# Optimization experiments

Measured on AMD Instinct MI355X. Metric: run time of the kernel, lower is better.

Reference implementation:

```python
import jax, jax.numpy as jnp
import numpy as np

NEG = -1e9

def setup_inputs() -> dict:
    key = jax.random.key(0)
    k1, k2, k3, k4, k5 = jax.random.split(key, 5)
    B, S, D = 4, 2048, 1024
    x = jax.random.normal(k1, (B, S, D), dtype=jnp.float32)
    Wq = jax.random.normal(k2, (D, D), dtype=jnp.float32) * (1.0 / np.sqrt(D))
    Wk = jax.random.normal(k3, (D, D), dtype=jnp.float32) * (1.0 / np.sqrt(D))
    Wv = jax.random.normal(k4, (D, D), dtype=jnp.float32) * (1.0 / np.sqrt(D))
    mask = jax.random.randint(k5, (B, S), 0, 2) > 0  # bool [B,S]
    return {"x": x, "Wq": Wq, "Wk": Wk, "Wv": Wv, "mask": mask}

def reference(x, Wq, Wk, Wv, mask):
    # x: [B,S,D]; single-head self-attention, scale = 1/sqrt(D)
    D = x.shape[-1]
    scale = 1.0 / D ** 0.5
    q = jnp.einsum('bsi,ij->bsj', x, Wq)
    k = jnp.einsum('bsi,ij->bsj', x, Wk)
    y = jnp.einsum('bsi,bzi->bsz', q, k) * scale  # [B,S,S]
    # additive mask: (~mask)[:, :, None] * -1e9 broadcasts over key axis
    m = (~mask).astype(jnp.float32)[:, :, None]
    y = y + m * NEG
    v = jnp.einsum('bsi,ij->bsj', x, Wv)
    attn = jax.nn.softmax(y, axis=-1)
    return jnp.einsum('bsz,bzi->bsi', attn, v)
```

## Files before the change

### kernel.cpp

```cpp
#include <hip/hip_runtime.h>

typedef __bf16 bf16x8 __attribute__((ext_vector_type(8)));
typedef float f32x4 __attribute__((ext_vector_type(4)));
typedef unsigned short u16;

__device__ __forceinline__ u16 f2bf(float f) {
    union { float f; unsigned u; } v; v.f = f;
    unsigned r = (v.u + 0x7FFFu + ((v.u >> 16) & 1u)) >> 16;
    return (u16)r;
}

__device__ __forceinline__ void fence_bar() {
    asm volatile("" ::: "memory");
    __builtin_amdgcn_s_barrier();
    asm volatile("" ::: "memory");
}

__global__ __launch_bounds__(256)
void normMask(const unsigned int* __restrict__ m, unsigned char* __restrict__ nm) {
    __shared__ int isByte;
    if (threadIdx.x == 0) isByte = 0;
    __syncthreads();
    int bad = 0;
    for (int i = threadIdx.x; i < 2048; i += 256) bad |= (m[i] > 1u);
    if (bad) atomicOr(&isByte, 1);
    __syncthreads();
    if (isByte) {
        const unsigned char* mb = (const unsigned char*)m;
        for (int i = threadIdx.x; i < 8192; i += 256) nm[i] = mb[i] ? 1 : 0;
    } else {
        for (int i = threadIdx.x; i < 8192; i += 256) nm[i] = (unsigned char)m[i];
    }
}

__global__ __launch_bounds__(256)
void transW(const float* __restrict__ Wq, const float* __restrict__ Wk,
            const float* __restrict__ Wv, u16* __restrict__ Wt) {
    __shared__ u16 tile[64][65];
    const float* W = blockIdx.z == 0 ? Wq : (blockIdx.z == 1 ? Wk : Wv);
    u16* out = Wt + (size_t)blockIdx.z * 1024 * 1024;
    int k0 = blockIdx.x * 64, n0 = blockIdx.y * 64;
    int t = threadIdx.x, cl = t & 63, rw = t >> 6;
    #pragma unroll
    for (int r = 0; r < 16; ++r) {
        int row = r * 4 + rw;
        tile[cl][row] = f2bf(W[(size_t)(k0 + row) * 1024 + n0 + cl]);
    }
    __syncthreads();
    #pragma unroll
    for (int r = 0; r < 16; ++r) {
        int row = r * 4 + rw;
        out[(size_t)(n0 + row) * 1024 + k0 + cl] = tile[row][cl];
    }
}

__global__ __launch_bounds__(256)
void convX(const float* __restrict__ x, u16* __restrict__ xb) {
    const size_t n4 = (size_t)8192 * 1024 / 4;
    for (size_t i = (size_t)blockIdx.x * 256 + threadIdx.x; i < n4; i += (size_t)gridDim.x * 256) {
        float4 v = ((const float4*)x)[i];
        ushort4 o = make_ushort4(f2bf(v.x), f2bf(v.y), f2bf(v.z), f2bf(v.w));
        ((ushort4*)xb)[i] = o;
    }
}

__global__ __launch_bounds__(256)
void transV(const u16* __restrict__ qkv, u16* __restrict__ vt) {
    __shared__ u16 tile[64][65];
    int b = blockIdx.z;
    int s0 = blockIdx.x * 64, d0 = blockIdx.y * 64;
    int t = threadIdx.x, cl = t & 63, rw = t >> 6;
    const u16* src = qkv + (size_t)b * 2048 * 3072 + 2048;
    #pragma unroll
    for (int r = 0; r < 16; ++r) {
        int row = r * 4 + rw;
        tile[cl][row] = src[(size_t)(s0 + row) * 3072 + d0 + cl];
    }
    __syncthreads();
    u16* dst = vt + (size_t)b * 1024 * 2048;
    #pragma unroll
    for (int r = 0; r < 16; ++r) {
        int row = r * 4 + rw;
        dst[(size_t)(d0 + row) * 2048 + s0 + cl] = tile[row][cl];
    }
}

template <int OUTV, int SWZ>
__global__ __launch_bounds__(512, 2)
void gemm8p(const u16* __restrict__ A_, int lda, size_t sA,
            const u16* __restrict__ B_, int ldb, size_t sB,
            void* __restrict__ Cout, int ldc, size_t sC,
            int kdim, int ntiles) {
    __shared__ u16 lds[65536];
    const u16* A = A_ + (size_t)blockIdx.z * sA;
    const u16* B = B_ + (size_t)blockIdx.z * sB;

    int bid = blockIdx.x;
    if (SWZ) {
        int cpx = gridDim.x >> 3;
        bid = (bid & 7) * cpx + (bid >> 3);
    }
    const int brow = (bid / ntiles) * 256, bcol = (bid % ntiles) * 256;

    const int t = threadIdx.x;
    const int w = t >> 6, l = t & 63;
    const int wr = w >> 2, wc = w & 3;

    const size_t gA_th = (size_t)(brow + w * 16 + (l >> 2)) * lda + (l & 3) * 8;
    const size_t gB_th = (size_t)(bcol + w * 16 + (l >> 2)) * ldb + (l & 3) * 8;
    const int stTh = w * 512 + l * 8;
    const int rA = (wr * 128 + (l & 15)) * 32 + (l >> 4) * 8;
    const int rB = 32768 + (wc * 64 + (l & 15)) * 32 + (l >> 4) * 8;

    auto lds3 = (__attribute__((address_space(3))) char*)lds;

    #define ISSUE(matB, kk, tt, buf) do {                                          \
        const u16* gp0 = ((matB) ? B : A) + ((matB) ? gB_th : gA_th)               \
                         + (size_t)(tt) * 64 + (size_t)(kk) * 32;                  \
        const int ldm_ = (matB) ? ldb : lda;                                       \
        const int lbase_ = ((matB) ? 32768 : 0) + (buf) * 16384 + (kk) * 8192 + stTh; \
        __builtin_amdgcn_global_load_lds(                                          \
            (const __attribute__((address_space(1))) void*)gp0,                    \
            (__attribute__((address_space(3))) void*)(lds3 + 2 * lbase_), 16, 0, 0); \
        __builtin_amdgcn_global_load_lds(                                          \
            (const __attribute__((address_space(1))) void*)(gp0 + (size_t)128 * ldm_), \
            (__attribute__((address_space(3))) void*)(lds3 + 2 * (lbase_ + 4096)), 16, 0, 0); \
    } while (0)

    f32x4 acc[8][4];
    #pragma unroll
    for (int m = 0; m < 8; ++m)
        #pragma unroll
        for (int n = 0; n < 4; ++n)
            acc[m][n] = (f32x4){0.f, 0.f, 0.f, 0.f};

    const int NT = kdim >> 6;

    ISSUE(0, 0, 0, 0); ISSUE(1, 0, 0, 0); ISSUE(0, 1, 0, 0); ISSUE(1, 1, 0, 0);
    if (NT > 1) {
        ISSUE(0, 0, 1, 1); ISSUE(1, 0, 1, 1);
        asm volatile("s_waitcnt vmcnt(4)" ::: "memory");
    } else {
        asm volatile("s_waitcnt vmcnt(0)" ::: "memory");
    }
    fence_bar();

    for (int tt = 0; tt < NT; ++tt) {
        const int c = tt & 1;
        const int ab = c * 16384;
        bf16x8 af[4], bfv[4];

        #pragma unroll
        for (int m = 0; m < 4; ++m) af[m] = *(const bf16x8*)&lds[ab + rA + m * 512];
        #pragma unroll
        for (int n = 0; n < 4; ++n) bfv[n] = *(const bf16x8*)&lds[ab + rB + n * 512];
        if (tt + 1 < NT) { ISSUE(0, 1, tt + 1, c ^ 1); ISSUE(1, 1, tt + 1, c ^ 1); }
        fence_bar();
        __builtin_amdgcn_s_setprio(1);
        #pragma unroll
        for (int m = 0; m < 4; ++m)
            #pragma unroll
            for (int n = 0; n < 4; ++n)
                acc[m][n] = __builtin_amdgcn_mfma_f32_16x16x32_bf16(af[m], bfv[n], acc[m][n], 0, 0, 0);
        __builtin_amdgcn_s_setprio(0);
        fence_bar();

        #pragma unroll
        for (int m = 0; m < 4; ++m) af[m] = *(const bf16x8*)&lds[ab + rA + (m + 4) * 512];
        fence_bar();
        __builtin_amdgcn_s_setprio(1);
        #pragma unroll
        for (int m = 0; m < 4; ++m)
            #pragma unroll
            for (int n = 0; n < 4; ++n)
                acc[m + 4][n] = __builtin_amdgcn_mfma_f32_16x16x32_bf16(af[m], bfv[n], acc[m + 4][n], 0, 0, 0);
        __builtin_amdgcn_s_setprio(0);
        fence_bar();

        #pragma unroll
        for (int m = 0; m < 4; ++m) af[m] = *(const bf16x8*)&lds[ab + 8192 + rA + m * 512];
        #pragma unroll
        for (int n = 0; n < 4; ++n) bfv[n] = *(const bf16x8*)&lds[ab + 8192 + rB + n * 512];
        if (tt + 2 < NT) ISSUE(0, 0, tt + 2, c);
        fence_bar();
        __builtin_amdgcn_s_setprio(1);
        #pragma unroll
        for (int m = 0; m < 4; ++m)
            #pragma unroll
            for (int n = 0; n < 4; ++n)
                acc[m][n] = __builtin_amdgcn_mfma_f32_16x16x32_bf16(af[m], bfv[n], acc[m][n], 0, 0, 0);
        __builtin_amdgcn_s_setprio(0);
        fence_bar();

        #pragma unroll
        for (int m = 0; m < 4; ++m) af[m] = *(const bf16x8*)&lds[ab + 8192 + rA + (m + 4) * 512];
        if (tt + 2 < NT) ISSUE(1, 0, tt + 2, c);
        fence_bar();
        __builtin_amdgcn_s_setprio(1);
        #pragma unroll
        for (int m = 0; m < 4; ++m)
            #pragma unroll
            for (int n = 0; n < 4; ++n)
                acc[m + 4][n] = __builtin_amdgcn_mfma_f32_16x16x32_bf16(af[m], bfv[n], acc[m + 4][n], 0, 0, 0);
        __builtin_amdgcn_s_setprio(0);
        if (tt + 2 < NT) asm volatile("s_waitcnt vmcnt(4)" ::: "memory");
        else             asm volatile("s_waitcnt vmcnt(0)" ::: "memory");
        fence_bar();
    }
    #undef ISSUE

    const int lr = (l >> 4) * 4, lc = l & 15;
    #pragma unroll
    for (int m = 0; m < 8; ++m) {
        #pragma unroll
        for (int n = 0; n < 4; ++n) {
            int rr = brow + wr * 128 + m * 16 + lr;
            int cc = bcol + wc * 64 + n * 16 + lc;
            #pragma unroll
            for (int j = 0; j < 4; ++j) {
                if constexpr (OUTV == 0)
                    ((u16*)Cout)[(size_t)blockIdx.z * sC + (size_t)(rr + j) * ldc + cc] = f2bf(acc[m][n][j]);
                else
                    ((float*)Cout)[(size_t)blockIdx.z * sC + (size_t)(rr + j) * ldc + cc] = acc[m][n][j];
            }
        }
    }
}

template <int OUTV>
__global__ __launch_bounds__(256, 2)
void gemm_bt(const u16* __restrict__ A0, int lda, size_t sA,
             const u16* __restrict__ B0, int ldb, size_t sB,
             void* __restrict__ Cout, int ldc, size_t sC, int kdim) {
    __shared__ u16 lA[128 * 64];
    __shared__ u16 lB[128 * 64];
    const u16* A = A0 + (size_t)blockIdx.z * sA;
    const u16* B = B0 + (size_t)blockIdx.z * sB;
    const int t = threadIdx.x;
    const int w = t >> 6, l = t & 63;
    const int wr = w >> 1, wc = w & 1;
    const int brow = blockIdx.x * 128, bcol = blockIdx.y * 128;
    const int rt = l >> 3;
    const int cb = (l & 7) * 8;

    auto ldsA3 = (__attribute__((address_space(3))) char*)lA;
    auto ldsB3 = (__attribute__((address_space(3))) char*)lB;

    f32x4 acc[4][4];
    #pragma unroll
    for (int m = 0; m < 4; ++m)
        #pragma unroll
        for (int n = 0; n < 4; ++n)
            acc[m][n] = (f32x4){0.f, 0.f, 0.f, 0.f};

    for (int k0 = 0; k0 < kdim; k0 += 64) {
        __syncthreads();
        #pragma unroll
        for (int p = 0; p < 4; ++p) {
            int chunk = p * 4 + w;
            const u16* ga = A + (size_t)(brow + chunk * 8 + rt) * lda + k0 + cb;
            __builtin_amdgcn_global_load_lds(
                (const __attribute__((address_space(1))) void*)ga,
                (__attribute__((address_space(3))) void*)(ldsA3 + chunk * 1024), 16, 0, 0);
            const u16* gb = B + (size_t)(bcol + chunk * 8 + rt) * ldb + k0 + cb;
            __builtin_amdgcn_global_load_lds(
                (const __attribute__((address_space(1))) void*)gb,
                (__attribute__((address_space(3))) void*)(ldsB3 + chunk * 1024), 16, 0, 0);
        }
        __syncthreads();
        #pragma unroll
        for (int kk = 0; kk < 2; ++kk) {
            bf16x8 af[4], bfv[4];
            #pragma unroll
            for (int m = 0; m < 4; ++m)
                af[m] = *(const bf16x8*)&lA[(wr * 64 + m * 16 + (l & 15)) * 64 + kk * 32 + (l >> 4) * 8];
            #pragma unroll
            for (int n = 0; n < 4; ++n)
                bfv[n] = *(const bf16x8*)&lB[(wc * 64 + n * 16 + (l & 15)) * 64 + kk * 32 + (l >> 4) * 8];
            #pragma unroll
            for (int m = 0; m < 4; ++m)
                #pragma unroll
                for (int n = 0; n < 4; ++n)
                    acc[m][n] = __builtin_amdgcn_mfma_f32_16x16x32_bf16(af[m], bfv[n], acc[m][n], 0, 0, 0);
        }
    }

    const int lrow = (l >> 4) * 4, lcol = l & 15;
    #pragma unroll
    for (int m = 0; m < 4; ++m) {
        #pragma unroll
        for (int n = 0; n < 4; ++n) {
            int rr = brow + wr * 64 + m * 16 + lrow;
            int cc = bcol + wc * 64 + n * 16 + lcol;
            #pragma unroll
            for (int j = 0; j < 4; ++j) {
                if constexpr (OUTV == 0)
                    ((u16*)Cout)[(size_t)blockIdx.z * sC + (size_t)(rr + j) * ldc + cc] = f2bf(acc[m][n][j]);
                else
                    ((float*)Cout)[(size_t)blockIdx.z * sC + (size_t)(rr + j) * ldc + cc] = acc[m][n][j];
            }
        }
    }
}

__global__ __launch_bounds__(256)
void softmax_rows(const float* __restrict__ S0, size_t sS, u16* __restrict__ P0, size_t sP,
                  const unsigned char* __restrict__ nm, int bbase) {
    const int row = blockIdx.x, t = threadIdx.x;
    const int b = bbase + blockIdx.z;
    const float* S = S0 + (size_t)blockIdx.z * sS;
    u16* dst = P0 + (size_t)blockIdx.z * sP + (size_t)row * 2048;
    if (nm[b * 2048 + row] == 0) {
        ushort4 u = make_ushort4(0x3A00, 0x3A00, 0x3A00, 0x3A00);
        ((ushort4*)dst)[t] = u;
        ((ushort4*)dst)[t + 256] = u;
        return;
    }
    const float4* src = (const float4*)(S + (size_t)row * 2048);
    float4 a = src[t], c = src[t + 256];
    float v[8] = {a.x, a.y, a.z, a.w, c.x, c.y, c.z, c.w};
    float mx = -1e30f;
    #pragma unroll
    for (int i = 0; i < 8; ++i) { v[i] *= 0.03125f; mx = fmaxf(mx, v[i]); }
    #pragma unroll
    for (int o = 32; o > 0; o >>= 1) mx = fmaxf(mx, __shfl_xor(mx, o));
    __shared__ float redm[4], reds[4];
    if ((t & 63) == 0) redm[t >> 6] = mx;
    __syncthreads();
    mx = fmaxf(fmaxf(redm[0], redm[1]), fmaxf(redm[2], redm[3]));
    float s = 0.f;
    #pragma unroll
    for (int i = 0; i < 8; ++i) { v[i] = expf(v[i] - mx); s += v[i]; }
    #pragma unroll
    for (int o = 32; o > 0; o >>= 1) s += __shfl_xor(s, o);
    if ((t & 63) == 0) reds[t >> 6] = s;
    __syncthreads();
    s = (reds[0] + reds[1]) + (reds[2] + reds[3]);
    float inv = 1.0f / s;
    ushort4 o0 = make_ushort4(f2bf(v[0] * inv), f2bf(v[1] * inv), f2bf(v[2] * inv), f2bf(v[3] * inv));
    ushort4 o1 = make_ushort4(f2bf(v[4] * inv), f2bf(v[5] * inv), f2bf(v[6] * inv), f2bf(v[7] * inv));
    ((ushort4*)dst)[t] = o0;
    ((ushort4*)dst)[t + 256] = o1;
}

extern "C" void kernel_launch(void* const* d_in, const int* in_sizes, int n_in,
                              void* d_out, int out_size, void* d_ws, size_t ws_size,
                              hipStream_t stream) {
    const float* x  = (const float*)d_in[0];
    const float* Wq = (const float*)d_in[1];
    const float* Wk = (const float*)d_in[2];
    const float* Wv = (const float*)d_in[3];
    const unsigned int* mask = (const unsigned int*)d_in[4];
    float* out = (float*)d_out;

    char* p = (char*)d_ws;
    u16* Wt  = (u16*)p;  p += (size_t)3072 * 1024 * 2;
    u16* xb  = (u16*)p;  p += (size_t)8192 * 1024 * 2;
    u16* qkv = (u16*)p;  p += (size_t)8192 * 3072 * 2;
    u16* vt  = (u16*)p;  p += (size_t)4 * 1024 * 2048 * 2;
    char* base = p;
    const size_t sizeS = (size_t)2048 * 2048 * 4;
    const size_t sizeP = (size_t)2048 * 2048 * 2;
    bool batched = ws_size >= (size_t)(base - (char*)d_ws) + 4 * (sizeS + sizeP) + 8192;

    float* S = (float*)base;
    u16* P;
    unsigned char* nm;
    if (batched) {
        P  = (u16*)(base + 4 * sizeS);
        nm = (unsigned char*)(base + 4 * (sizeS + sizeP));
    } else {
        P  = (u16*)(base + sizeS);
        nm = (unsigned char*)(base + sizeS + sizeP);
    }

    normMask<<<1, 256, 0, stream>>>(mask, nm);
    transW<<<dim3(16, 16, 3), 256, 0, stream>>>(Wq, Wk, Wv, Wt);
    convX<<<2048, 256, 0, stream>>>(x, xb);
    gemm8p<0, 1><<<dim3(384, 1, 1), 512, 0, stream>>>(
        xb, 1024, 0, Wt, 1024, 0, qkv, 3072, 0, 1024, 12);
    transV<<<dim3(32, 16, 4), 256, 0, stream>>>(qkv, vt);

    if (batched) {
        gemm8p<1, 0><<<dim3(64, 1, 4), 512, 0, stream>>>(
            qkv, 3072, (size_t)2048 * 3072, qkv + 1024, 3072, (size_t)2048 * 3072,
            S, 2048, (size_t)2048 * 2048, 1024, 8);
        softmax_rows<<<dim3(2048, 1, 4), 256, 0, stream>>>(
            S, (size_t)2048 * 2048, P, (size_t)2048 * 2048, nm, 0);
        gemm_bt<2><<<dim3(16, 8, 4), 256, 0, stream>>>(
            P, 2048, (size_t)2048 * 2048, vt, 2048, (size_t)1024 * 2048,
            out, 1024, (size_t)2048 * 1024, 2048);
    } else {
        for (int b = 0; b < 4; ++b) {
            const u16* Qb = qkv + (size_t)b * 2048 * 3072;
            gemm8p<1, 0><<<dim3(64, 1, 1), 512, 0, stream>>>(
                Qb, 3072, 0, Qb + 1024, 3072, 0, S, 2048, 0, 1024, 8);
            softmax_rows<<<dim3(2048, 1, 1), 256, 0, stream>>>(S, 0, P, 0, nm, b);
            gemm_bt<2><<<dim3(16, 8, 1), 256, 0, stream>>>(
                P, 2048, 0, vt + (size_t)b * 1024 * 2048, 2048, 0,
                out + (size_t)b * 2048 * 1024, 1024, 0, 2048);
        }
    }
}
```

Before: 211.0 us.

## Use XOR-swizzled 64-wide LDS tiles and single-stage prefetch in gemm8p

The GEMM's LDS tile layout changes from two 32-column k-halves to full 64-column rows with an XOR swizzle on the 16-byte slots, so the MFMA fragment reads avoid LDS bank conflicts. The global-to-LDS load schedule is reworked into a one-tile-ahead prefetch spread across the four compute phases, with a vmcnt wait at the first and last phase. The XCD block-index swizzle for the QKV projection GEMM is removed, which may reduce L2 locality across dies. The change also shortens how far ahead loads are issued, so latency hiding could get worse.

```diff
diff --git a/kernel.cpp b/kernel.cpp
--- a/kernel.cpp
+++ b/kernel.cpp
@@ -85,7 +85,7 @@
     }
 }
 
-template <int OUTV, int SWZ>
+template <int OUTV>
 __global__ __launch_bounds__(512, 2)
 void gemm8p(const u16* __restrict__ A_, int lda, size_t sA,
             const u16* __restrict__ B_, int ldb, size_t sB,
@@ -95,36 +95,29 @@
     const u16* A = A_ + (size_t)blockIdx.z * sA;
     const u16* B = B_ + (size_t)blockIdx.z * sB;
 
-    int bid = blockIdx.x;
-    if (SWZ) {
-        int cpx = gridDim.x >> 3;
-        bid = (bid & 7) * cpx + (bid >> 3);
-    }
+    const int bid = blockIdx.x;
     const int brow = (bid / ntiles) * 256, bcol = (bid % ntiles) * 256;
-
     const int t = threadIdx.x;
     const int w = t >> 6, l = t & 63;
     const int wr = w >> 2, wc = w & 3;
 
-    const size_t gA_th = (size_t)(brow + w * 16 + (l >> 2)) * lda + (l & 3) * 8;
-    const size_t gB_th = (size_t)(bcol + w * 16 + (l >> 2)) * ldb + (l & 3) * 8;
-    const int stTh = w * 512 + l * 8;
-    const int rA = (wr * 128 + (l & 15)) * 32 + (l >> 4) * 8;
-    const int rB = 32768 + (wc * 64 + (l & 15)) * 32 + (l >> 4) * 8;
+    const int srow = t >> 3;
+    const int sslot = (t & 7) ^ (srow & 7);
+    const int aBase = (wr * 128 + (l & 15)) * 64;
+    const int bBase = 32768 + (wc * 64 + (l & 15)) * 64;
+    const int cx0 = (((l >> 4)) ^ (l & 7)) * 8;
+    const int cx1 = (((l >> 4) + 4) ^ (l & 7)) * 8;
 
     auto lds3 = (__attribute__((address_space(3))) char*)lds;
 
-    #define ISSUE(matB, kk, tt, buf) do {                                          \
-        const u16* gp0 = ((matB) ? B : A) + ((matB) ? gB_th : gA_th)               \
-                         + (size_t)(tt) * 64 + (size_t)(kk) * 32;                  \
-        const int ldm_ = (matB) ? ldb : lda;                                       \
-        const int lbase_ = ((matB) ? 32768 : 0) + (buf) * 16384 + (kk) * 8192 + stTh; \
+    #define ISSUE(matB, q, tt, buf) do {                                           \
+        const u16* gsrc = ((matB) ? B : A)                                         \
+            + (size_t)(((matB) ? bcol : brow) + (q) * 64 + srow) * ((matB) ? ldb : lda) \
+            + (size_t)(tt) * 64 + sslot * 8;                                       \
+        const int dst_ = ((matB) ? 32768 : 0) + (buf) * 16384 + (q) * 4096 + t * 8; \
         __builtin_amdgcn_global_load_lds(                                          \
-            (const __attribute__((address_space(1))) void*)gp0,                    \
-            (__attribute__((address_space(3))) void*)(lds3 + 2 * lbase_), 16, 0, 0); \
-        __builtin_amdgcn_global_load_lds(                                          \
-            (const __attribute__((address_space(1))) void*)(gp0 + (size_t)128 * ldm_), \
-            (__attribute__((address_space(3))) void*)(lds3 + 2 * (lbase_ + 4096)), 16, 0, 0); \
+            (const __attribute__((address_space(1))) void*)gsrc,                   \
+            (__attribute__((address_space(3))) void*)(lds3 + 2 * dst_), 16, 0, 0); \
     } while (0)
 
     f32x4 acc[8][4];
@@ -136,25 +129,28 @@
 
     const int NT = kdim >> 6;
 
-    ISSUE(0, 0, 0, 0); ISSUE(1, 0, 0, 0); ISSUE(0, 1, 0, 0); ISSUE(1, 1, 0, 0);
-    if (NT > 1) {
-        ISSUE(0, 0, 1, 1); ISSUE(1, 0, 1, 1);
-        asm volatile("s_waitcnt vmcnt(4)" ::: "memory");
-    } else {
-        asm volatile("s_waitcnt vmcnt(0)" ::: "memory");
-    }
+    ISSUE(1, 0, 0, 0); ISSUE(1, 1, 0, 0); ISSUE(1, 2, 0, 0); ISSUE(1, 3, 0, 0);
+    ISSUE(0, 0, 0, 0); ISSUE(0, 2, 0, 0); ISSUE(0, 1, 0, 0); ISSUE(0, 3, 0, 0);
+    asm volatile("s_waitcnt vmcnt(2)" ::: "memory");
     fence_bar();
 
     for (int tt = 0; tt < NT; ++tt) {
         const int c = tt & 1;
         const int ab = c * 16384;
+        const int nb = c ^ 1;
+        const bool pf = (tt + 1 < NT);
         bf16x8 af[4], bfv[4];
 
         #pragma unroll
-        for (int m = 0; m < 4; ++m) af[m] = *(const bf16x8*)&lds[ab + rA + m * 512];
-        #pragma unroll
-        for (int n = 0; n < 4; ++n) bfv[n] = *(const bf16x8*)&lds[ab + rB + n * 512];
-        if (tt + 1 < NT) { ISSUE(0, 1, tt + 1, c ^ 1); ISSUE(1, 1, tt + 1, c ^ 1); }
+        for (int m = 0; m < 4; ++m) af[m] = *(const bf16x8*)&lds[ab + aBase + m * 1024 + cx0];
+        #pragma unroll
+        for (int n = 0; n < 4; ++n) bfv[n] = *(const bf16x8*)&lds[ab + bBase + n * 1024 + cx0];
+        if (pf) {
+            ISSUE(1, 0, tt + 1, nb); ISSUE(1, 1, tt + 1, nb);
+            asm volatile("s_waitcnt vmcnt(2)" ::: "memory");
+        } else {
+            asm volatile("s_waitcnt vmcnt(0)" ::: "memory");
+        }
         fence_bar();
         __builtin_amdgcn_s_setprio(1);
         #pragma unroll
@@ -166,7 +162,8 @@
         fence_bar();
 
         #pragma unroll
-        for (int m = 0; m < 4; ++m) af[m] = *(const bf16x8*)&lds[ab + rA + (m + 4) * 512];
+        for (int m = 0; m < 4; ++m) af[m] = *(const bf16x8*)&lds[ab + aBase + (m + 4) * 1024 + cx0];
+        if (pf) { ISSUE(1, 2, tt + 1, nb); ISSUE(1, 3, tt + 1, nb); }
         fence_bar();
         __builtin_amdgcn_s_setprio(1);
         #pragma unroll
@@ -178,10 +175,10 @@
         fence_bar();
 
         #pragma unroll
-        for (int m = 0; m < 4; ++m) af[m] = *(const bf16x8*)&lds[ab + 8192 + rA + m * 512];
-        #pragma unroll
-        for (int n = 0; n < 4; ++n) bfv[n] = *(const bf16x8*)&lds[ab + 8192 + rB + n * 512];
-        if (tt + 2 < NT) ISSUE(0, 0, tt + 2, c);
+        for (int m = 0; m < 4; ++m) af[m] = *(const bf16x8*)&lds[ab + aBase + m * 1024 + cx1];
+        #pragma unroll
+        for (int n = 0; n < 4; ++n) bfv[n] = *(const bf16x8*)&lds[ab + bBase + n * 1024 + cx1];
+        if (pf) { ISSUE(0, 0, tt + 1, nb); ISSUE(0, 2, tt + 1, nb); }
         fence_bar();
         __builtin_amdgcn_s_setprio(1);
         #pragma unroll
@@ -193,8 +190,13 @@
         fence_bar();
 
         #pragma unroll
-        for (int m = 0; m < 4; ++m) af[m] = *(const bf16x8*)&lds[ab + 8192 + rA + (m + 4) * 512];
-        if (tt + 2 < NT) ISSUE(1, 0, tt + 2, c);
+        for (int m = 0; m < 4; ++m) af[m] = *(const bf16x8*)&lds[ab + aBase + (m + 4) * 1024 + cx1];
+        if (pf) {
+            ISSUE(0, 1, tt + 1, nb); ISSUE(0, 3, tt + 1, nb);
+            asm volatile("s_waitcnt vmcnt(2)" ::: "memory");
+        } else {
+            asm volatile("s_waitcnt vmcnt(0)" ::: "memory");
+        }
         fence_bar();
         __builtin_amdgcn_s_setprio(1);
         #pragma unroll
@@ -203,8 +205,6 @@
             for (int n = 0; n < 4; ++n)
                 acc[m + 4][n] = __builtin_amdgcn_mfma_f32_16x16x32_bf16(af[m], bfv[n], acc[m + 4][n], 0, 0, 0);
         __builtin_amdgcn_s_setprio(0);
-        if (tt + 2 < NT) asm volatile("s_waitcnt vmcnt(4)" ::: "memory");
-        else             asm volatile("s_waitcnt vmcnt(0)" ::: "memory");
         fence_bar();
     }
     #undef ISSUE
@@ -377,12 +377,12 @@
     normMask<<<1, 256, 0, stream>>>(mask, nm);
     transW<<<dim3(16, 16, 3), 256, 0, stream>>>(Wq, Wk, Wv, Wt);
     convX<<<2048, 256, 0, stream>>>(x, xb);
-    gemm8p<0, 1><<<dim3(384, 1, 1), 512, 0, stream>>>(
+    gemm8p<0><<<dim3(384, 1, 1), 512, 0, stream>>>(
         xb, 1024, 0, Wt, 1024, 0, qkv, 3072, 0, 1024, 12);
     transV<<<dim3(32, 16, 4), 256, 0, stream>>>(qkv, vt);
 
     if (batched) {
-        gemm8p<1, 0><<<dim3(64, 1, 4), 512, 0, stream>>>(
+        gemm8p<1><<<dim3(64, 1, 4), 512, 0, stream>>>(
             qkv, 3072, (size_t)2048 * 3072, qkv + 1024, 3072, (size_t)2048 * 3072,
             S, 2048, (size_t)2048 * 2048, 1024, 8);
         softmax_rows<<<dim3(2048, 1, 4), 256, 0, stream>>>(
@@ -393,7 +393,7 @@
     } else {
         for (int b = 0; b < 4; ++b) {
             const u16* Qb = qkv + (size_t)b * 2048 * 3072;
-            gemm8p<1, 0><<<dim3(64, 1, 1), 512, 0, stream>>>(
+            gemm8p<1><<<dim3(64, 1, 1), 512, 0, stream>>>(
                 Qb, 3072, 0, Qb + 1024, 3072, 0, S, 2048, 0, 1024, 8);
             softmax_rows<<<dim3(2048, 1, 1), 256, 0, stream>>>(S, 0, P, 0, nm, b);
             gemm_bt<2><<<dim3(16, 8, 1), 256, 0, stream>>>(
```

After: 201.3 us. -4.6%, faster.
